# Optimization experiments

Hardware: AMD Instinct MI355X
Metric: run time of the kernel (lower is better)

## Reference

```python
import jax, jax.numpy as jnp
import numpy as np

EPS = 1e-5  # eqx.nn.LayerNorm default


def _layer_norm(x, w, b):
    m = x.mean(-1, keepdims=True)
    v = ((x - m) ** 2).mean(-1, keepdims=True)
    return (x - m) / jnp.sqrt(v + EPS) * w + b


def _s4_block(x, nw, nb, lre, lim, bre, bim, cre, cim, d, lstep, ow, ob, o2w, o2b):
    # x: [L, H]. One SequenceBlock: LayerNorm -> S4 recurrence (lax.scan) -> GELU -> GLU-style gated linear -> residual.
    skip = x
    h = _layer_norm(x, nw, nb)
    Lam = lre + 1j * lim                      # [H, N] complex diagonal state matrix
    step = jnp.exp(lstep)[:, None]            # [H, 1] per-channel timescale
    BL = 1.0 / (1.0 - (step / 2.0) * Lam)     # bilinear discretization
    Abar = BL * (1.0 + (step / 2.0) * Lam)    # [H, N]
    Bbar = BL * step * (bre + 1j * bim)       # [H, N]
    C = cre + 1j * cim                        # [H, N]

    def scan_fn(state, u):                    # state: [H, N] complex, u: [H]
        new = Abar * state + Bbar * u[:, None]
        y = 2.0 * jnp.sum(C * new, axis=-1).real + d * u
        return new, y

    init = jnp.zeros(Abar.shape, Abar.dtype)  # cell.init_state
    _, y = jax.lax.scan(scan_fn, init, h)     # [L, H]
    y = jax.nn.gelu(y)
    y = (y @ ow.T + ob) * jax.nn.sigmoid(y @ o2w.T + o2b)
    return skip + y


def setup_inputs() -> dict:
    key = jax.random.key(0)
    L, IN, OUT, H, N, NL = 2048, 4, 3, 512, 32, 4
    ks = jax.random.split(key, 16)
    return {
        "x": jax.random.normal(ks[0], (L, IN), jnp.float32),
        "enc_w": jax.random.normal(ks[1], (H, IN), jnp.float32) / np.sqrt(IN),
        "enc_b": jnp.zeros((H,), jnp.float32),
        "dec_w": jax.random.normal(ks[2], (OUT, H), jnp.float32) / np.sqrt(H),
        "dec_b": jnp.zeros((OUT,), jnp.float32),
        "norm_w": jnp.ones((NL, H), jnp.float32),
        "norm_b": jnp.zeros((NL, H), jnp.float32),
        "lam_re": -0.5 - jax.random.uniform(ks[3], (NL, H, N), jnp.float32),  # stable (Re < 0)
        "lam_im": np.pi * jax.random.normal(ks[4], (NL, H, N), jnp.float32),
        "b_re": jax.random.normal(ks[5], (NL, H, N), jnp.float32) / np.sqrt(N),
        "b_im": jax.random.normal(ks[6], (NL, H, N), jnp.float32) / np.sqrt(N),
        "c_re": jax.random.normal(ks[7], (NL, H, N), jnp.float32) / np.sqrt(N),
        "c_im": jax.random.normal(ks[8], (NL, H, N), jnp.float32) / np.sqrt(N),
        "d": jax.random.normal(ks[9], (NL, H), jnp.float32),
        "log_step": float(np.log(1e-3)) + float(np.log(1e-1) - np.log(1e-3)) * jax.random.uniform(ks[10], (NL, H), jnp.float32),
        "out_w": jax.random.normal(ks[11], (NL, H, H), jnp.float32) / np.sqrt(H),
        "out_b": jnp.zeros((NL, H), jnp.float32),
        "out2_w": jax.random.normal(ks[12], (NL, H, H), jnp.float32) / np.sqrt(H),
        "out2_b": jnp.zeros((NL, H), jnp.float32),
    }


def reference(x, enc_w, enc_b, dec_w, dec_b, norm_w, norm_b, lam_re, lam_im, b_re, b_im, c_re, c_im, d, log_step, out_w, out_b, out2_w, out2_b):
    h = x @ enc_w.T + enc_b                   # encoder: [L, IN] -> [L, H]
    for i in range(norm_w.shape[0]):          # fixed small n_layers loop
        h = _s4_block(h, norm_w[i], norm_b[i], lam_re[i], lam_im[i], b_re[i], b_im[i],
                      c_re[i], c_im[i], d[i], log_step[i], out_w[i], out_b[i], out2_w[i], out2_b[i])
    return h @ dec_w.T + dec_b                # decoder: [L, H] -> [L, OUT]
```

## Files before the change

kernel.cpp:

```cpp
#include <hip/hip_runtime.h>
#include <hip/hip_bf16.h>
#include <math.h>

#define LSEQ 2048
#define HD   512
#define NST  32
#define LC   32
#define NCHK 64
#define SUP  8
#define NSUP 8
#define HH   (HD * HD)

typedef __bf16 bf16;
typedef __bf16 bf16x8 __attribute__((ext_vector_type(8)));
typedef float  floatx4 __attribute__((ext_vector_type(4)));

__device__ __forceinline__ float wave_reduce_add(float v) {
#pragma unroll
    for (int m = 32; m; m >>= 1) v += __shfl_xor(v, m, 64);
    return v;
}

__device__ __forceinline__ float gelu_tanh(float x) {
    float z = 0.7978845608028654f * (x + 0.044715f * x * x * x);
    float e = __expf(2.f * z);
    float th = 1.f - 2.f / (e + 1.f);
    return 0.5f * x * (1.f + th);
}

__device__ __forceinline__ void make_ab(float lre, float lim, float step,
                                        float br0, float bi0,
                                        float& ar, float& ai, float& br, float& bi) {
    float s2 = 0.5f * step;
    float dr = 1.f - s2 * lre, di = -s2 * lim;
    float inv = 1.f / (dr * dr + di * di);
    float blr = dr * inv, bli = -di * inv;
    float nr = 1.f + s2 * lre, ni = s2 * lim;
    ar = blr * nr - bli * ni;
    ai = blr * ni + bli * nr;
    float tr = step * br0, ti = step * bi0;
    br = blr * tr - bli * ti;
    bi = blr * ti + bli * tr;
}

__global__ __launch_bounds__(256) void prep_kernel(
    const float* __restrict__ lre, const float* __restrict__ lim,
    const float* __restrict__ bre, const float* __restrict__ bim,
    const float* __restrict__ cre, const float* __restrict__ cim,
    const float* __restrict__ ls,
    float2* __restrict__ cA, float2* __restrict__ cB,
    float2* __restrict__ cC, float2* __restrict__ cAp) {
    int tid = blockIdx.x * 256 + threadIdx.x;
    int lay = tid >> 14, rem = tid & 16383;
    int ch = rem >> 5, n = rem & 31;
    int src = tid;
    float step = __expf(ls[lay * HD + ch]);
    float ar, ai, br, bi;
    make_ab(lre[src], lim[src], step, bre[src], bim[src], ar, ai, br, bi);
    float xr = ar, xi = ai;
#pragma unroll
    for (int q = 0; q < 5; ++q) { float tt = xr * xr - xi * xi; xi = 2.f * xr * xi; xr = tt; }
    int dst = (lay * NST + n) * HD + ch;
    cA[dst]  = make_float2(ar, ai);
    cB[dst]  = make_float2(br, bi);
    cC[dst]  = make_float2(2.f * cre[src], 2.f * cim[src]);
    cAp[dst] = make_float2(xr, xi);
}

__global__ __launch_bounds__(256) void cvt_kernel(
    const float* __restrict__ ow, const float* __restrict__ o2w,
    bf16* __restrict__ wb) {
    const float* src = blockIdx.y ? o2w : ow;
    bf16* dst = wb + blockIdx.y * (4 * HH);
    int i = (blockIdx.x * 256 + threadIdx.x) * 8;
    float4 a = *(const float4*)(src + i);
    float4 b = *(const float4*)(src + i + 4);
    bf16x8 o;
    o[0] = (bf16)a.x; o[1] = (bf16)a.y; o[2] = (bf16)a.z; o[3] = (bf16)a.w;
    o[4] = (bf16)b.x; o[5] = (bf16)b.y; o[6] = (bf16)b.z; o[7] = (bf16)b.w;
    *(bf16x8*)(dst + i) = o;
}

__global__ __launch_bounds__(256) void enc_kernel(
    const float* __restrict__ x, const float* __restrict__ w,
    const float* __restrict__ b, float* __restrict__ h) {
    int idx = blockIdx.x * 256 + threadIdx.x;
    int t = idx >> 9, i = idx & (HD - 1);
    float acc = b[i];
    float4 xv = *(const float4*)(x + t * 4);
    float4 wv = *(const float4*)(w + i * 4);
    acc = fmaf(xv.x, wv.x, acc);
    acc = fmaf(xv.y, wv.y, acc);
    acc = fmaf(xv.z, wv.z, acc);
    acc = fmaf(xv.w, wv.w, acc);
    h[idx] = acc;
}

__global__ __launch_bounds__(256) void ln_kernel(
    const float* __restrict__ h, float* __restrict__ hn,
    const float* __restrict__ w, const float* __restrict__ b) {
    int wv = threadIdx.x >> 6, lane = threadIdx.x & 63;
    int row = blockIdx.x * 4 + wv;
    const float* hp = h + row * HD + lane * 8;
    float v[8];
    *(float4*)(v)     = *(const float4*)(hp);
    *(float4*)(v + 4) = *(const float4*)(hp + 4);
    float s = 0.f;
#pragma unroll
    for (int e = 0; e < 8; ++e) s += v[e];
    s = wave_reduce_add(s);
    float m = s * (1.f / HD);
    float q = 0.f;
#pragma unroll
    for (int e = 0; e < 8; ++e) { float d = v[e] - m; q += d * d; }
    q = wave_reduce_add(q);
    float rstd = rsqrtf(q * (1.f / HD) + 1e-5f);
    float w8[8], b8[8];
    *(float4*)(w8)     = *(const float4*)(w + lane * 8);
    *(float4*)(w8 + 4) = *(const float4*)(w + lane * 8 + 4);
    *(float4*)(b8)     = *(const float4*)(b + lane * 8);
    *(float4*)(b8 + 4) = *(const float4*)(b + lane * 8 + 4);
    float o[8];
#pragma unroll
    for (int e = 0; e < 8; ++e)
        o[e] = (v[e] - m) * rstd * w8[e] + b8[e];
    float* op = hn + row * HD + lane * 8;
    *(float4*)op       = *(float4*)o;
    *(float4*)(op + 4) = *(float4*)(o + 4);
}

__global__ __launch_bounds__(256, 2) void p1_kernel(
    const float* __restrict__ u,
    const float2* __restrict__ cA, const float2* __restrict__ cB,
    float2* __restrict__ f, int lay) {
    __shared__ float tile[4 * LC * 16];
    int tid = threadIdx.x;
    int lane = tid & 63, w = tid >> 6;
    int chl = lane & 15;
    int ch = blockIdx.x * 16 + chl;
    int sub = lane >> 4;
    int chunk = blockIdx.y * 4 + w;
    int t0 = blockIdx.y * 4 * LC;
    const float* ub = u + (size_t)t0 * HD + blockIdx.x * 16;
#pragma unroll
    for (int r = 0; r < 8; ++r) {
        int idx = r * 256 + tid;
        tile[idx] = ub[(idx >> 4) * HD + (idx & 15)];
    }
    int cbase = (lay * NST + sub * 8) * HD + ch;
    float aR[8], aI[8], bR[8], bI[8];
#pragma unroll
    for (int j = 0; j < 8; ++j) {
        float2 t = cA[cbase + j * HD]; aR[j] = t.x; aI[j] = t.y;
        t = cB[cbase + j * HD];        bR[j] = t.x; bI[j] = t.y;
    }
    float sr[8], si[8];
#pragma unroll
    for (int j = 0; j < 8; ++j) { sr[j] = 0.f; si[j] = 0.f; }
    __syncthreads();
    const float* tp = tile + (w * LC) * 16 + chl;
#pragma unroll 4
    for (int t = 0; t < LC; ++t) {
        float uu = tp[t * 16];
#pragma unroll
        for (int j = 0; j < 8; ++j) {
            float nr = fmaf(aR[j], sr[j], fmaf(-aI[j], si[j], bR[j] * uu));
            float ni = fmaf(aI[j], sr[j], fmaf( aR[j], si[j], bI[j] * uu));
            sr[j] = nr; si[j] = ni;
        }
    }
    float2* fp = f + (chunk * NST + sub * 8) * HD + ch;
#pragma unroll
    for (int j = 0; j < 8; ++j) fp[j * HD] = make_float2(sr[j], si[j]);
}

__global__ __launch_bounds__(256) void p2a_kernel(
    float2* __restrict__ f, const float2* __restrict__ cAp, int lay) {
    int tg = blockIdx.x * 256 + threadIdx.x;
    int ch = tg & 511;
    int ns = tg >> 9;
    int n = ns & 31, sup = ns >> 5;
    float2 ap = cAp[(lay * NST + n) * HD + ch];
    float2* fp = f + ((sup * SUP) * NST + n) * HD + ch;
    float sr = 0.f, si = 0.f;
#pragma unroll
    for (int j = 0; j < SUP; ++j) {
        float2 v = fp[(size_t)j * NST * HD];
        float nr = fmaf(ap.x, sr, fmaf(-ap.y, si, v.x));
        float ni = fmaf(ap.y, sr, fmaf( ap.x, si, v.y));
        sr = nr; si = ni;
        fp[(size_t)j * NST * HD] = make_float2(sr, si);
    }
}

__global__ __launch_bounds__(256) void p2b_kernel(
    float2* __restrict__ f, const float2* __restrict__ cAp, int lay) {
    int tg = blockIdx.x * 256 + threadIdx.x;
    int ch = tg & 511, n = tg >> 9;
    float2 ap = cAp[(lay * NST + n) * HD + ch];
    float xr = ap.x, xi = ap.y;
#pragma unroll
    for (int q = 0; q < 3; ++q) { float tt = xr * xr - xi * xi; xi = 2.f * xr * xi; xr = tt; }
    float2* fp = f + ((SUP - 1) * NST + n) * HD + ch;
    const size_t stride = (size_t)SUP * NST * HD;
    float sr = 0.f, si = 0.f;
#pragma unroll
    for (int k = 0; k < NSUP; ++k) {
        float2 v = fp[k * stride];
        float nr = fmaf(xr, sr, fmaf(-xi, si, v.x));
        float ni = fmaf(xi, sr, fmaf( xr, si, v.y));
        sr = nr; si = ni;
        fp[k * stride] = make_float2(sr, si);
    }
}

__global__ __launch_bounds__(256) void p2c_kernel(
    float2* __restrict__ f, const float2* __restrict__ cAp, int lay) {
    int tg = blockIdx.x * 256 + threadIdx.x;
    int ch = tg & 511;
    int ns = tg >> 9;
    int n = ns & 31, sup = ns >> 5;
    if (sup == 0) return;
    float2 ap = cAp[(lay * NST + n) * HD + ch];
    float2 S = f[((sup * SUP - 1) * NST + n) * HD + ch];
    float2* fp = f + ((sup * SUP) * NST + n) * HD + ch;
    float wr = ap.x, wi = ap.y;
#pragma unroll
    for (int j = 0; j < SUP - 1; ++j) {
        float2 v = fp[(size_t)j * NST * HD];
        v.x += wr * S.x - wi * S.y;
        v.y += wr * S.y + wi * S.x;
        fp[(size_t)j * NST * HD] = v;
        float nwr = wr * ap.x - wi * ap.y;
        float nwi = wr * ap.y + wi * ap.x;
        wr = nwr; wi = nwi;
    }
}

__global__ __launch_bounds__(256, 2) void p3_kernel(
    const float* __restrict__ u, const float2* __restrict__ f,
    const float2* __restrict__ cA, const float2* __restrict__ cB,
    const float2* __restrict__ cC, const float* __restrict__ d_p,
    bf16* __restrict__ g, int lay) {
    __shared__ float tile[4 * LC * 16];
    int tid = threadIdx.x;
    int lane = tid & 63, w = tid >> 6;
    int chl = lane & 15;
    int ch = blockIdx.x * 16 + chl;
    int sub = lane >> 4;
    int chunk = blockIdx.y * 4 + w;
    int t0 = blockIdx.y * 4 * LC;
    const float* ub = u + (size_t)t0 * HD + blockIdx.x * 16;
#pragma unroll
    for (int r = 0; r < 8; ++r) {
        int idx = r * 256 + tid;
        tile[idx] = ub[(idx >> 4) * HD + (idx & 15)];
    }
    int cbase = (lay * NST + sub * 8) * HD + ch;
    float aR[8], aI[8], bR[8], bI[8], cR[8], cI[8];
#pragma unroll
    for (int j = 0; j < 8; ++j) {
        float2 t = cA[cbase + j * HD]; aR[j] = t.x; aI[j] = t.y;
        t = cB[cbase + j * HD];        bR[j] = t.x; bI[j] = t.y;
        t = cC[cbase + j * HD];        cR[j] = t.x; cI[j] = t.y;
    }
    float dch = d_p[lay * HD + ch];
    float sr[8], si[8];
    if (chunk > 0) {
        const float2* ip = f + ((chunk - 1) * NST + sub * 8) * HD + ch;
#pragma unroll
        for (int j = 0; j < 8; ++j) { float2 v = ip[j * HD]; sr[j] = v.x; si[j] = v.y; }
    } else {
#pragma unroll
        for (int j = 0; j < 8; ++j) { sr[j] = 0.f; si[j] = 0.f; }
    }
    __syncthreads();
    const float* tp = tile + (w * LC) * 16 + chl;
    bf16* gp = g + (size_t)chunk * LC * HD + ch;
#pragma unroll 4
    for (int t = 0; t < LC; ++t) {
        float uu = tp[t * 16];
        float p = 0.f;
#pragma unroll
        for (int j = 0; j < 8; ++j) {
            float nr = fmaf(aR[j], sr[j], fmaf(-aI[j], si[j], bR[j] * uu));
            float ni = fmaf(aI[j], sr[j], fmaf( aR[j], si[j], bI[j] * uu));
            sr[j] = nr; si[j] = ni;
            p = fmaf(cR[j], nr, fmaf(-cI[j], ni, p));
        }
        p += __shfl_xor(p, 16);
        p += __shfl_xor(p, 32);
        float y = fmaf(dch, uu, p);
        if (sub == 0) gp[t * HD] = (bf16)gelu_tanh(y);
    }
}

__global__ __launch_bounds__(256) void mm_kernel(
    const bf16* __restrict__ A,
    const bf16* __restrict__ W1,
    const bf16* __restrict__ W2,
    const float* __restrict__ bias1, const float* __restrict__ bias2,
    float* __restrict__ Hio) {
    const int w = threadIdx.x >> 6, lane = threadIdx.x & 63;
    const int wm = w >> 1, wn = w & 1;
    const int mBase = blockIdx.y * 64 + wm * 32;
    const int nBase = blockIdx.x * 64 + wn * 32;
    const int lrow = lane & 15, quad = lane >> 4;

    floatx4 acc1[2][2] = {{{0.f,0.f,0.f,0.f},{0.f,0.f,0.f,0.f}},{{0.f,0.f,0.f,0.f},{0.f,0.f,0.f,0.f}}};
    floatx4 acc2[2][2] = {{{0.f,0.f,0.f,0.f},{0.f,0.f,0.f,0.f}},{{0.f,0.f,0.f,0.f},{0.f,0.f,0.f,0.f}}};

    for (int k0 = 0; k0 < HD; k0 += 32) {
        int kk = k0 + quad * 8;
        bf16x8 a0 = *(const bf16x8*)(A + (mBase + lrow) * HD + kk);
        bf16x8 a1 = *(const bf16x8*)(A + (mBase + 16 + lrow) * HD + kk);
        bf16x8 p0 = *(const bf16x8*)(W1 + (nBase + lrow) * HD + kk);
        bf16x8 p1 = *(const bf16x8*)(W1 + (nBase + 16 + lrow) * HD + kk);
        bf16x8 q0 = *(const bf16x8*)(W2 + (nBase + lrow) * HD + kk);
        bf16x8 q1 = *(const bf16x8*)(W2 + (nBase + 16 + lrow) * HD + kk);
        acc1[0][0] = __builtin_amdgcn_mfma_f32_16x16x32_bf16(a0, p0, acc1[0][0], 0, 0, 0);
        acc1[0][1] = __builtin_amdgcn_mfma_f32_16x16x32_bf16(a0, p1, acc1[0][1], 0, 0, 0);
        acc1[1][0] = __builtin_amdgcn_mfma_f32_16x16x32_bf16(a1, p0, acc1[1][0], 0, 0, 0);
        acc1[1][1] = __builtin_amdgcn_mfma_f32_16x16x32_bf16(a1, p1, acc1[1][1], 0, 0, 0);
        acc2[0][0] = __builtin_amdgcn_mfma_f32_16x16x32_bf16(a0, q0, acc2[0][0], 0, 0, 0);
        acc2[0][1] = __builtin_amdgcn_mfma_f32_16x16x32_bf16(a0, q1, acc2[0][1], 0, 0, 0);
        acc2[1][0] = __builtin_amdgcn_mfma_f32_16x16x32_bf16(a1, q0, acc2[1][0], 0, 0, 0);
        acc2[1][1] = __builtin_amdgcn_mfma_f32_16x16x32_bf16(a1, q1, acc2[1][1], 0, 0, 0);
    }

#pragma unroll
    for (int fm = 0; fm < 2; ++fm)
#pragma unroll
        for (int fn = 0; fn < 2; ++fn) {
            int j = nBase + fn * 16 + lrow;
            float bb1 = bias1[j], bb2 = bias2[j];
#pragma unroll
            for (int r = 0; r < 4; ++r) {
                int t = mBase + fm * 16 + quad * 4 + r;
                float z1 = acc1[fm][fn][r] + bb1;
                float z2 = acc2[fm][fn][r] + bb2;
                float val = z1 / (1.f + __expf(-z2));
                Hio[t * HD + j] += val;
            }
        }
}

__global__ __launch_bounds__(192) void dec_kernel(
    const float* __restrict__ h, const float* __restrict__ w,
    const float* __restrict__ b, float* __restrict__ out) {
    int j = threadIdx.x >> 6, lane = threadIdx.x & 63;
    int t = blockIdx.x;
    const float* hp = h + t * HD + lane * 8;
    float v[8];
    *(float4*)(v)     = *(const float4*)(hp);
    *(float4*)(v + 4) = *(const float4*)(hp + 4);
    float w8[8];
    *(float4*)(w8)     = *(const float4*)(w + j * HD + lane * 8);
    *(float4*)(w8 + 4) = *(const float4*)(w + j * HD + lane * 8 + 4);
    float s = 0.f;
#pragma unroll
    for (int e = 0; e < 8; ++e) s = fmaf(v[e], w8[e], s);
    s = wave_reduce_add(s);
    if (lane == 0) out[t * 3 + j] = s + b[j];
}

extern "C" void kernel_launch(void* const* d_in, const int* in_sizes, int n_in,
                              void* d_out, int out_size, void* d_ws, size_t ws_size,
                              hipStream_t stream) {
    const float* x   = (const float*)d_in[0];
    const float* ew  = (const float*)d_in[1];
    const float* eb  = (const float*)d_in[2];
    const float* dw  = (const float*)d_in[3];
    const float* db  = (const float*)d_in[4];
    const float* nw  = (const float*)d_in[5];
    const float* nb  = (const float*)d_in[6];
    const float* lre = (const float*)d_in[7];
    const float* lim = (const float*)d_in[8];
    const float* bre = (const float*)d_in[9];
    const float* bim = (const float*)d_in[10];
    const float* cre = (const float*)d_in[11];
    const float* cim = (const float*)d_in[12];
    const float* dd  = (const float*)d_in[13];
    const float* ls  = (const float*)d_in[14];
    const float* ow  = (const float*)d_in[15];
    const float* ob  = (const float*)d_in[16];
    const float* o2w = (const float*)d_in[17];
    const float* o2b = (const float*)d_in[18];

    char* ws = (char*)d_ws;
    float*  h   = (float*)ws;
    float*  hn  = (float*)(ws + (4  << 20));
    float2* f   = (float2*)(ws + (8  << 20));
    bf16*   g   = (bf16*)(ws + (24 << 20));
    bf16*   wb  = (bf16*)(ws + (26 << 20));
    float2* cA  = (float2*)(ws + (30 << 20));
    float2* cB  = (float2*)(ws + (30 << 20) + (512 << 10));
    float2* cC  = (float2*)(ws + (31 << 20));
    float2* cAp = (float2*)(ws + (31 << 20) + (512 << 10));

    prep_kernel<<<256, 256, 0, stream>>>(lre, lim, bre, bim, cre, cim, ls, cA, cB, cC, cAp);
    cvt_kernel<<<dim3(4 * HH / (256 * 8), 2), 256, 0, stream>>>(ow, o2w, wb);
    enc_kernel<<<LSEQ * HD / 256, 256, 0, stream>>>(x, ew, eb, h);
    for (int lay = 0; lay < 4; ++lay) {
        int oH = lay * HD;
        ln_kernel<<<LSEQ / 4, 256, 0, stream>>>(h, hn, nw + oH, nb + oH);
        p1_kernel<<<dim3(HD / 16, NCHK / 4), 256, 0, stream>>>(hn, cA, cB, f, lay);
        p2a_kernel<<<512, 256, 0, stream>>>(f, cAp, lay);
        p2b_kernel<<<64, 256, 0, stream>>>(f, cAp, lay);
        p2c_kernel<<<512, 256, 0, stream>>>(f, cAp, lay);
        p3_kernel<<<dim3(HD / 16, NCHK / 4), 256, 0, stream>>>(hn, f, cA, cB, cC, dd, g, lay);
        mm_kernel<<<dim3(HD / 64, LSEQ / 64), 256, 0, stream>>>(
            g, wb + lay * HH, wb + 4 * HH + lay * HH, ob + oH, o2b + oH, h);
    }
    dec_kernel<<<LSEQ, 192, 0, stream>>>(h, dw, db, (float*)d_out);
}
```

Before: 317.0 us.

## Fuse setup kernels, defer LayerNorm into scan tiles, simplify chunk scan, retile GEMM

Merges the encoder, weight conversion and parameter prep into one setup launch. LayerNorm now only computes per-row mean and rstd, and the normalization is applied while loading tiles in p1 and p3, so the hn buffer is gone. The three-kernel hierarchical cross-chunk scan becomes one sequential 64-step scan per state using the chunk-power A^32. The GEMM uses smaller 64x32 tiles over a 1D grid of 512 blocks to get more blocks in flight. Fewer launches and less traffic are traded for a longer serial dependency in p2 and less reuse per GEMM tile.

```diff
diff --git a/kernel.cpp b/kernel.cpp
--- a/kernel.cpp
+++ b/kernel.cpp
@@ -7,9 +7,8 @@
 #define NST  32
 #define LC   32
 #define NCHK 64
-#define SUP  8
-#define NSUP 8
 #define HH   (HD * HD)
+#define NTHR 256
 
 typedef __bf16 bf16;
 typedef __bf16 bf16x8 __attribute__((ext_vector_type(8)));
@@ -43,65 +42,61 @@
     bi = blr * ti + bli * tr;
 }
 
-__global__ __launch_bounds__(256) void prep_kernel(
+__global__ __launch_bounds__(256) void setup_kernel(
+    const float* __restrict__ x,   const float* __restrict__ ew,
+    const float* __restrict__ eb,  const float* __restrict__ ow,
+    const float* __restrict__ o2w,
     const float* __restrict__ lre, const float* __restrict__ lim,
     const float* __restrict__ bre, const float* __restrict__ bim,
     const float* __restrict__ cre, const float* __restrict__ cim,
     const float* __restrict__ ls,
+    float* __restrict__ h, bf16* __restrict__ wb,
     float2* __restrict__ cA, float2* __restrict__ cB,
     float2* __restrict__ cC, float2* __restrict__ cAp) {
-    int tid = blockIdx.x * 256 + threadIdx.x;
-    int lay = tid >> 14, rem = tid & 16383;
-    int ch = rem >> 5, n = rem & 31;
-    int src = tid;
-    float step = __expf(ls[lay * HD + ch]);
-    float ar, ai, br, bi;
-    make_ab(lre[src], lim[src], step, bre[src], bim[src], ar, ai, br, bi);
-    float xr = ar, xi = ai;
-#pragma unroll
-    for (int q = 0; q < 5; ++q) { float tt = xr * xr - xi * xi; xi = 2.f * xr * xi; xr = tt; }
-    int dst = (lay * NST + n) * HD + ch;
-    cA[dst]  = make_float2(ar, ai);
-    cB[dst]  = make_float2(br, bi);
-    cC[dst]  = make_float2(2.f * cre[src], 2.f * cim[src]);
-    cAp[dst] = make_float2(xr, xi);
-}
-
-__global__ __launch_bounds__(256) void cvt_kernel(
-    const float* __restrict__ ow, const float* __restrict__ o2w,
-    bf16* __restrict__ wb) {
-    const float* src = blockIdx.y ? o2w : ow;
-    bf16* dst = wb + blockIdx.y * (4 * HH);
-    int i = (blockIdx.x * 256 + threadIdx.x) * 8;
-    float4 a = *(const float4*)(src + i);
-    float4 b = *(const float4*)(src + i + 4);
-    bf16x8 o;
-    o[0] = (bf16)a.x; o[1] = (bf16)a.y; o[2] = (bf16)a.z; o[3] = (bf16)a.w;
-    o[4] = (bf16)b.x; o[5] = (bf16)b.y; o[6] = (bf16)b.z; o[7] = (bf16)b.w;
-    *(bf16x8*)(dst + i) = o;
-}
-
-__global__ __launch_bounds__(256) void enc_kernel(
-    const float* __restrict__ x, const float* __restrict__ w,
-    const float* __restrict__ b, float* __restrict__ h) {
-    int idx = blockIdx.x * 256 + threadIdx.x;
-    int t = idx >> 9, i = idx & (HD - 1);
-    float acc = b[i];
-    float4 xv = *(const float4*)(x + t * 4);
-    float4 wv = *(const float4*)(w + i * 4);
-    acc = fmaf(xv.x, wv.x, acc);
-    acc = fmaf(xv.y, wv.y, acc);
-    acc = fmaf(xv.z, wv.z, acc);
-    acc = fmaf(xv.w, wv.w, acc);
-    h[idx] = acc;
-}
-
-__global__ __launch_bounds__(256) void ln_kernel(
-    const float* __restrict__ h, float* __restrict__ hn,
-    const float* __restrict__ w, const float* __restrict__ b) {
+    int bid = blockIdx.x, tid = threadIdx.x;
+    if (bid < 4096) {
+        int idx = bid * 256 + tid;
+        int t = idx >> 9, i = idx & (HD - 1);
+        float4 xv = *(const float4*)(x + t * 4);
+        float4 wv = *(const float4*)(ew + i * 4);
+        float acc = eb[i];
+        acc = fmaf(xv.x, wv.x, acc); acc = fmaf(xv.y, wv.y, acc);
+        acc = fmaf(xv.z, wv.z, acc); acc = fmaf(xv.w, wv.w, acc);
+        h[idx] = acc;
+    } else if (bid < 5120) {
+        int b2 = bid - 4096;
+        const float* src = (b2 >= 512) ? o2w : ow;
+        bf16* dst = wb + (b2 >= 512 ? 4 * HH : 0);
+        int i = ((b2 & 511) * 256 + tid) * 8;
+        float4 a = *(const float4*)(src + i);
+        float4 b = *(const float4*)(src + i + 4);
+        bf16x8 o;
+        o[0] = (bf16)a.x; o[1] = (bf16)a.y; o[2] = (bf16)a.z; o[3] = (bf16)a.w;
+        o[4] = (bf16)b.x; o[5] = (bf16)b.y; o[6] = (bf16)b.z; o[7] = (bf16)b.w;
+        *(bf16x8*)(dst + i) = o;
+    } else {
+        int tg = (bid - 5120) * 256 + tid;
+        int lay = tg >> 14, rem = tg & 16383;
+        int ch = rem >> 5, n = rem & 31;
+        float step = __expf(ls[lay * HD + ch]);
+        float ar, ai, br, bi;
+        make_ab(lre[tg], lim[tg], step, bre[tg], bim[tg], ar, ai, br, bi);
+        float xr = ar, xi = ai;
+#pragma unroll
+        for (int q = 0; q < 5; ++q) { float tt = xr * xr - xi * xi; xi = 2.f * xr * xi; xr = tt; }
+        int dst = (lay * NST + n) * HD + ch;
+        cA[dst]  = make_float2(ar, ai);
+        cB[dst]  = make_float2(br, bi);
+        cC[dst]  = make_float2(2.f * cre[tg], 2.f * cim[tg]);
+        cAp[dst] = make_float2(xr, xi);
+    }
+}
+
+__global__ __launch_bounds__(256) void lnstat_kernel(
+    const float* __restrict__ h, float2* __restrict__ stats) {
     int wv = threadIdx.x >> 6, lane = threadIdx.x & 63;
     int row = blockIdx.x * 4 + wv;
-    const float* hp = h + row * HD + lane * 8;
+    const float* hp = h + (size_t)row * HD + lane * 8;
     float v[8];
     *(float4*)(v)     = *(const float4*)(hp);
     *(float4*)(v + 4) = *(const float4*)(hp + 4);
@@ -115,38 +110,47 @@
     for (int e = 0; e < 8; ++e) { float d = v[e] - m; q += d * d; }
     q = wave_reduce_add(q);
     float rstd = rsqrtf(q * (1.f / HD) + 1e-5f);
-    float w8[8], b8[8];
-    *(float4*)(w8)     = *(const float4*)(w + lane * 8);
-    *(float4*)(w8 + 4) = *(const float4*)(w + lane * 8 + 4);
-    *(float4*)(b8)     = *(const float4*)(b + lane * 8);
-    *(float4*)(b8 + 4) = *(const float4*)(b + lane * 8 + 4);
-    float o[8];
-#pragma unroll
-    for (int e = 0; e < 8; ++e)
-        o[e] = (v[e] - m) * rstd * w8[e] + b8[e];
-    float* op = hn + row * HD + lane * 8;
-    *(float4*)op       = *(float4*)o;
-    *(float4*)(op + 4) = *(float4*)(o + 4);
+    if (lane == 0) stats[row] = make_float2(m, rstd);
+}
+
+__device__ __forceinline__ void load_norm_tile(
+    float* tile, const float* __restrict__ h, const float2* __restrict__ stats,
+    const float* __restrict__ nwp, const float* __restrict__ nbp,
+    int bx, int by, int tid) {
+    const float* ub = h + (size_t)(by * 4 * LC) * HD + bx * 16;
+    const float2* st = stats + by * 4 * LC;
+    const float* wp = nwp + bx * 16;
+    const float* bp = nbp + bx * 16;
+#pragma unroll
+    for (int r = 0; r < 2; ++r) {
+        int i = r * NTHR + tid;
+        int tr = i >> 2, c4 = (i & 3) * 4;
+        float4 hv = *(const float4*)(ub + (size_t)tr * HD + c4);
+        float2 s2 = st[tr];
+        float4 gv = *(const float4*)(wp + c4);
+        float4 bv = *(const float4*)(bp + c4);
+        float4 o;
+        o.x = (hv.x - s2.x) * s2.y * gv.x + bv.x;
+        o.y = (hv.y - s2.x) * s2.y * gv.y + bv.y;
+        o.z = (hv.z - s2.x) * s2.y * gv.z + bv.z;
+        o.w = (hv.w - s2.x) * s2.y * gv.w + bv.w;
+        *(float4*)(tile + tr * 16 + c4) = o;
+    }
 }
 
 __global__ __launch_bounds__(256, 2) void p1_kernel(
-    const float* __restrict__ u,
+    const float* __restrict__ h, const float2* __restrict__ stats,
+    const float* __restrict__ nwp, const float* __restrict__ nbp,
     const float2* __restrict__ cA, const float2* __restrict__ cB,
     float2* __restrict__ f, int lay) {
     __shared__ float tile[4 * LC * 16];
     int tid = threadIdx.x;
     int lane = tid & 63, w = tid >> 6;
-    int chl = lane & 15;
-    int ch = blockIdx.x * 16 + chl;
-    int sub = lane >> 4;
-    int chunk = blockIdx.y * 4 + w;
-    int t0 = blockIdx.y * 4 * LC;
-    const float* ub = u + (size_t)t0 * HD + blockIdx.x * 16;
-#pragma unroll
-    for (int r = 0; r < 8; ++r) {
-        int idx = r * 256 + tid;
-        tile[idx] = ub[(idx >> 4) * HD + (idx & 15)];
-    }
+    int chl = lane & 15, sub = lane >> 4;
+    int bx = blockIdx.x, by = blockIdx.y;
+    int ch = bx * 16 + chl;
+    int chunk = by * 4 + w;
+    load_norm_tile(tile, h, stats, nwp, nbp, bx, by, tid);
     int cbase = (lay * NST + sub * 8) * HD + ch;
     float aR[8], aI[8], bR[8], bI[8];
 #pragma unroll
@@ -169,93 +173,44 @@
             sr[j] = nr; si[j] = ni;
         }
     }
-    float2* fp = f + (chunk * NST + sub * 8) * HD + ch;
-#pragma unroll
-    for (int j = 0; j < 8; ++j) fp[j * HD] = make_float2(sr[j], si[j]);
-}
-
-__global__ __launch_bounds__(256) void p2a_kernel(
-    float2* __restrict__ f, const float2* __restrict__ cAp, int lay) {
-    int tg = blockIdx.x * 256 + threadIdx.x;
-    int ch = tg & 511;
-    int ns = tg >> 9;
-    int n = ns & 31, sup = ns >> 5;
-    float2 ap = cAp[(lay * NST + n) * HD + ch];
-    float2* fp = f + ((sup * SUP) * NST + n) * HD + ch;
-    float sr = 0.f, si = 0.f;
-#pragma unroll
-    for (int j = 0; j < SUP; ++j) {
-        float2 v = fp[(size_t)j * NST * HD];
-        float nr = fmaf(ap.x, sr, fmaf(-ap.y, si, v.x));
-        float ni = fmaf(ap.y, sr, fmaf( ap.x, si, v.y));
-        sr = nr; si = ni;
-        fp[(size_t)j * NST * HD] = make_float2(sr, si);
-    }
-}
-
-__global__ __launch_bounds__(256) void p2b_kernel(
+    float2* fp = f + (size_t)(chunk * NST + sub * 8) * HD + ch;
+#pragma unroll
+    for (int j = 0; j < 8; ++j) fp[(size_t)j * HD] = make_float2(sr[j], si[j]);
+}
+
+__global__ __launch_bounds__(256) void p2_kernel(
     float2* __restrict__ f, const float2* __restrict__ cAp, int lay) {
     int tg = blockIdx.x * 256 + threadIdx.x;
     int ch = tg & 511, n = tg >> 9;
     float2 ap = cAp[(lay * NST + n) * HD + ch];
-    float xr = ap.x, xi = ap.y;
-#pragma unroll
-    for (int q = 0; q < 3; ++q) { float tt = xr * xr - xi * xi; xi = 2.f * xr * xi; xr = tt; }
-    float2* fp = f + ((SUP - 1) * NST + n) * HD + ch;
-    const size_t stride = (size_t)SUP * NST * HD;
+    float2* fp = f + (size_t)n * HD + ch;
+    const size_t cs = (size_t)NST * HD;
     float sr = 0.f, si = 0.f;
-#pragma unroll
-    for (int k = 0; k < NSUP; ++k) {
-        float2 v = fp[k * stride];
-        float nr = fmaf(xr, sr, fmaf(-xi, si, v.x));
-        float ni = fmaf(xi, sr, fmaf( xr, si, v.y));
+#pragma unroll 8
+    for (int c = 0; c < NCHK; ++c) {
+        float2 v = fp[c * cs];
+        float nr = fmaf(ap.x, sr, fmaf(-ap.y, si, v.x));
+        float ni = fmaf(ap.y, sr, fmaf( ap.x, si, v.y));
         sr = nr; si = ni;
-        fp[k * stride] = make_float2(sr, si);
-    }
-}
-
-__global__ __launch_bounds__(256) void p2c_kernel(
-    float2* __restrict__ f, const float2* __restrict__ cAp, int lay) {
-    int tg = blockIdx.x * 256 + threadIdx.x;
-    int ch = tg & 511;
-    int ns = tg >> 9;
-    int n = ns & 31, sup = ns >> 5;
-    if (sup == 0) return;
-    float2 ap = cAp[(lay * NST + n) * HD + ch];
-    float2 S = f[((sup * SUP - 1) * NST + n) * HD + ch];
-    float2* fp = f + ((sup * SUP) * NST + n) * HD + ch;
-    float wr = ap.x, wi = ap.y;
-#pragma unroll
-    for (int j = 0; j < SUP - 1; ++j) {
-        float2 v = fp[(size_t)j * NST * HD];
-        v.x += wr * S.x - wi * S.y;
-        v.y += wr * S.y + wi * S.x;
-        fp[(size_t)j * NST * HD] = v;
-        float nwr = wr * ap.x - wi * ap.y;
-        float nwi = wr * ap.y + wi * ap.x;
-        wr = nwr; wi = nwi;
+        fp[c * cs] = make_float2(sr, si);
     }
 }
 
 __global__ __launch_bounds__(256, 2) void p3_kernel(
-    const float* __restrict__ u, const float2* __restrict__ f,
+    const float* __restrict__ h, const float2* __restrict__ stats,
+    const float* __restrict__ nwp, const float* __restrict__ nbp,
+    const float2* __restrict__ f,
     const float2* __restrict__ cA, const float2* __restrict__ cB,
     const float2* __restrict__ cC, const float* __restrict__ d_p,
     bf16* __restrict__ g, int lay) {
     __shared__ float tile[4 * LC * 16];
     int tid = threadIdx.x;
     int lane = tid & 63, w = tid >> 6;
-    int chl = lane & 15;
-    int ch = blockIdx.x * 16 + chl;
-    int sub = lane >> 4;
-    int chunk = blockIdx.y * 4 + w;
-    int t0 = blockIdx.y * 4 * LC;
-    const float* ub = u + (size_t)t0 * HD + blockIdx.x * 16;
-#pragma unroll
-    for (int r = 0; r < 8; ++r) {
-        int idx = r * 256 + tid;
-        tile[idx] = ub[(idx >> 4) * HD + (idx & 15)];
-    }
+    int chl = lane & 15, sub = lane >> 4;
+    int bx = blockIdx.x, by = blockIdx.y;
+    int ch = bx * 16 + chl;
+    int chunk = by * 4 + w;
+    load_norm_tile(tile, h, stats, nwp, nbp, bx, by, tid);
     int cbase = (lay * NST + sub * 8) * HD + ch;
     float aR[8], aI[8], bR[8], bI[8], cR[8], cI[8];
 #pragma unroll
@@ -267,9 +222,9 @@
     float dch = d_p[lay * HD + ch];
     float sr[8], si[8];
     if (chunk > 0) {
-        const float2* ip = f + ((chunk - 1) * NST + sub * 8) * HD + ch;
-#pragma unroll
-        for (int j = 0; j < 8; ++j) { float2 v = ip[j * HD]; sr[j] = v.x; si[j] = v.y; }
+        const float2* ip = f + (size_t)((chunk - 1) * NST + sub * 8) * HD + ch;
+#pragma unroll
+        for (int j = 0; j < 8; ++j) { float2 v = ip[(size_t)j * HD]; sr[j] = v.x; si[j] = v.y; }
     } else {
 #pragma unroll
         for (int j = 0; j < 8; ++j) { sr[j] = 0.f; si[j] = 0.f; }
@@ -291,11 +246,11 @@
         p += __shfl_xor(p, 16);
         p += __shfl_xor(p, 32);
         float y = fmaf(dch, uu, p);
-        if (sub == 0) gp[t * HD] = (bf16)gelu_tanh(y);
-    }
-}
-
-__global__ __launch_bounds__(256) void mm_kernel(
+        if (sub == 0) gp[(size_t)t * HD] = (bf16)gelu_tanh(y);
+    }
+}
+
+__global__ __launch_bounds__(256, 2) void mm_kernel(
     const bf16* __restrict__ A,
     const bf16* __restrict__ W1,
     const bf16* __restrict__ W2,
@@ -303,45 +258,34 @@
     float* __restrict__ Hio) {
     const int w = threadIdx.x >> 6, lane = threadIdx.x & 63;
     const int wm = w >> 1, wn = w & 1;
-    const int mBase = blockIdx.y * 64 + wm * 32;
-    const int nBase = blockIdx.x * 64 + wn * 32;
+    const int bm = blockIdx.x >> 4, bn = blockIdx.x & 15;
+    const int mW = bm * 64 + wm * 32;
+    const int nW = bn * 32 + wn * 16;
     const int lrow = lane & 15, quad = lane >> 4;
 
-    floatx4 acc1[2][2] = {{{0.f,0.f,0.f,0.f},{0.f,0.f,0.f,0.f}},{{0.f,0.f,0.f,0.f},{0.f,0.f,0.f,0.f}}};
-    floatx4 acc2[2][2] = {{{0.f,0.f,0.f,0.f},{0.f,0.f,0.f,0.f}},{{0.f,0.f,0.f,0.f},{0.f,0.f,0.f,0.f}}};
-
+    floatx4 acc1[2] = {{0.f,0.f,0.f,0.f},{0.f,0.f,0.f,0.f}};
+    floatx4 acc2[2] = {{0.f,0.f,0.f,0.f},{0.f,0.f,0.f,0.f}};
     for (int k0 = 0; k0 < HD; k0 += 32) {
         int kk = k0 + quad * 8;
-        bf16x8 a0 = *(const bf16x8*)(A + (mBase + lrow) * HD + kk);
-        bf16x8 a1 = *(const bf16x8*)(A + (mBase + 16 + lrow) * HD + kk);
-        bf16x8 p0 = *(const bf16x8*)(W1 + (nBase + lrow) * HD + kk);
-        bf16x8 p1 = *(const bf16x8*)(W1 + (nBase + 16 + lrow) * HD + kk);
-        bf16x8 q0 = *(const bf16x8*)(W2 + (nBase + lrow) * HD + kk);
-        bf16x8 q1 = *(const bf16x8*)(W2 + (nBase + 16 + lrow) * HD + kk);
-        acc1[0][0] = __builtin_amdgcn_mfma_f32_16x16x32_bf16(a0, p0, acc1[0][0], 0, 0, 0);
-        acc1[0][1] = __builtin_amdgcn_mfma_f32_16x16x32_bf16(a0, p1, acc1[0][1], 0, 0, 0);
-        acc1[1][0] = __builtin_amdgcn_mfma_f32_16x16x32_bf16(a1, p0, acc1[1][0], 0, 0, 0);
-        acc1[1][1] = __builtin_amdgcn_mfma_f32_16x16x32_bf16(a1, p1, acc1[1][1], 0, 0, 0);
-        acc2[0][0] = __builtin_amdgcn_mfma_f32_16x16x32_bf16(a0, q0, acc2[0][0], 0, 0, 0);
-        acc2[0][1] = __builtin_amdgcn_mfma_f32_16x16x32_bf16(a0, q1, acc2[0][1], 0, 0, 0);
-        acc2[1][0] = __builtin_amdgcn_mfma_f32_16x16x32_bf16(a1, q0, acc2[1][0], 0, 0, 0);
-        acc2[1][1] = __builtin_amdgcn_mfma_f32_16x16x32_bf16(a1, q1, acc2[1][1], 0, 0, 0);
-    }
-
+        bf16x8 a0 = *(const bf16x8*)(A + (size_t)(mW + lrow) * HD + kk);
+        bf16x8 a1 = *(const bf16x8*)(A + (size_t)(mW + 16 + lrow) * HD + kk);
+        bf16x8 p0 = *(const bf16x8*)(W1 + (size_t)(nW + lrow) * HD + kk);
+        bf16x8 q0 = *(const bf16x8*)(W2 + (size_t)(nW + lrow) * HD + kk);
+        acc1[0] = __builtin_amdgcn_mfma_f32_16x16x32_bf16(a0, p0, acc1[0], 0, 0, 0);
+        acc1[1] = __builtin_amdgcn_mfma_f32_16x16x32_bf16(a1, p0, acc1[1], 0, 0, 0);
+        acc2[0] = __builtin_amdgcn_mfma_f32_16x16x32_bf16(a0, q0, acc2[0], 0, 0, 0);
+        acc2[1] = __builtin_amdgcn_mfma_f32_16x16x32_bf16(a1, q0, acc2[1], 0, 0, 0);
+    }
+    int jj = nW + lrow;
+    float bb1 = bias1[jj], bb2 = bias2[jj];
 #pragma unroll
     for (int fm = 0; fm < 2; ++fm)
 #pragma unroll
-        for (int fn = 0; fn < 2; ++fn) {
-            int j = nBase + fn * 16 + lrow;
-            float bb1 = bias1[j], bb2 = bias2[j];
-#pragma unroll
-            for (int r = 0; r < 4; ++r) {
-                int t = mBase + fm * 16 + quad * 4 + r;
-                float z1 = acc1[fm][fn][r] + bb1;
-                float z2 = acc2[fm][fn][r] + bb2;
-                float val = z1 / (1.f + __expf(-z2));
-                Hio[t * HD + j] += val;
-            }
+        for (int r = 0; r < 4; ++r) {
+            int t = mW + fm * 16 + quad * 4 + r;
+            float z1 = acc1[fm][r] + bb1;
+            float z2 = acc2[fm][r] + bb2;
+            Hio[(size_t)t * HD + jj] += z1 / (1.f + __expf(-z2));
         }
 }
 
@@ -350,7 +294,7 @@
     const float* __restrict__ b, float* __restrict__ out) {
     int j = threadIdx.x >> 6, lane = threadIdx.x & 63;
     int t = blockIdx.x;
-    const float* hp = h + t * HD + lane * 8;
+    const float* hp = h + (size_t)t * HD + lane * 8;
     float v[8];
     *(float4*)(v)     = *(const float4*)(hp);
     *(float4*)(v + 4) = *(const float4*)(hp + 4);
@@ -388,28 +332,28 @@
     const float* o2b = (const float*)d_in[18];
 
     char* ws = (char*)d_ws;
-    float*  h   = (float*)ws;
-    float*  hn  = (float*)(ws + (4  << 20));
-    float2* f   = (float2*)(ws + (8  << 20));
-    bf16*   g   = (bf16*)(ws + (24 << 20));
-    bf16*   wb  = (bf16*)(ws + (26 << 20));
-    float2* cA  = (float2*)(ws + (30 << 20));
-    float2* cB  = (float2*)(ws + (30 << 20) + (512 << 10));
-    float2* cC  = (float2*)(ws + (31 << 20));
-    float2* cAp = (float2*)(ws + (31 << 20) + (512 << 10));
-
-    prep_kernel<<<256, 256, 0, stream>>>(lre, lim, bre, bim, cre, cim, ls, cA, cB, cC, cAp);
-    cvt_kernel<<<dim3(4 * HH / (256 * 8), 2), 256, 0, stream>>>(ow, o2w, wb);
-    enc_kernel<<<LSEQ * HD / 256, 256, 0, stream>>>(x, ew, eb, h);
+    float*  h     = (float*)ws;
+    float2* f     = (float2*)(ws + (4  << 20));
+    bf16*   g     = (bf16*)(ws + (16 << 20));
+    bf16*   wb    = (bf16*)(ws + (18 << 20));
+    float2* cA    = (float2*)(ws + (22 << 20));
+    float2* cB    = (float2*)(ws + (22 << 20) + (512 << 10));
+    float2* cC    = (float2*)(ws + (23 << 20));
+    float2* cAp   = (float2*)(ws + (23 << 20) + (512 << 10));
+    float2* stats = (float2*)(ws + (24 << 20));
+
+    setup_kernel<<<5376, 256, 0, stream>>>(x, ew, eb, ow, o2w,
+                                           lre, lim, bre, bim, cre, cim, ls,
+                                           h, wb, cA, cB, cC, cAp);
     for (int lay = 0; lay < 4; ++lay) {
         int oH = lay * HD;
-        ln_kernel<<<LSEQ / 4, 256, 0, stream>>>(h, hn, nw + oH, nb + oH);
-        p1_kernel<<<dim3(HD / 16, NCHK / 4), 256, 0, stream>>>(hn, cA, cB, f, lay);
-        p2a_kernel<<<512, 256, 0, stream>>>(f, cAp, lay);
-        p2b_kernel<<<64, 256, 0, stream>>>(f, cAp, lay);
-        p2c_kernel<<<512, 256, 0, stream>>>(f, cAp, lay);
-        p3_kernel<<<dim3(HD / 16, NCHK / 4), 256, 0, stream>>>(hn, f, cA, cB, cC, dd, g, lay);
-        mm_kernel<<<dim3(HD / 64, LSEQ / 64), 256, 0, stream>>>(
+        lnstat_kernel<<<LSEQ / 4, 256, 0, stream>>>(h, stats);
+        p1_kernel<<<dim3(HD / 16, NCHK / 4), 256, 0, stream>>>(
+            h, stats, nw + oH, nb + oH, cA, cB, f, lay);
+        p2_kernel<<<64, 256, 0, stream>>>(f, cAp, lay);
+        p3_kernel<<<dim3(HD / 16, NCHK / 4), 256, 0, stream>>>(
+            h, stats, nw + oH, nb + oH, f, cA, cB, cC, dd, g, lay);
+        mm_kernel<<<512, 256, 0, stream>>>(
             g, wb + lay * HH, wb + 4 * HH + lay * HH, ob + oH, o2b + oH, h);
     }
     dec_kernel<<<LSEQ, 192, 0, stream>>>(h, dw, db, (float*)d_out);
```

After: 305.6 us. 3.6% less time.
